# Kernel optimization log

Hardware: AMD Instinct MI355X
Metric: run time of the kernel (lower is better)

## Reference

```python
import jax, jax.numpy as jnp
import numpy as np

EPS = 1e-5

def _bn(x, g, b, m, v):
    # inference-mode batchnorm with moving statistics
    return (x - m) * jax.lax.rsqrt(v + EPS) * g + b

def setup_inputs() -> dict:
    key = jax.random.key(0)
    ks = jax.random.split(key, 12)
    t, b, s, hu = 512, 64, 1024, 1024
    d_in = s + hu
    si = jax.random.normal(ks[0], (b, s), dtype=jnp.float32)
    h = jax.random.normal(ks[1], (t, b, hu), dtype=jnp.float32)
    W0 = jax.random.normal(ks[2], (d_in, 10), dtype=jnp.float32) * 0.02
    b0 = jnp.zeros((10,), jnp.float32)
    g0 = jnp.ones((10,), jnp.float32)
    be0 = jnp.zeros((10,), jnp.float32)
    m0 = jax.random.normal(ks[3], (10,), dtype=jnp.float32) * 0.1
    v0 = jax.random.uniform(ks[4], (10,), dtype=jnp.float32) + 0.5
    W1 = jax.random.normal(ks[5], (10, 5), dtype=jnp.float32) * 0.3
    b1 = jnp.zeros((5,), jnp.float32)
    g1 = jnp.ones((5,), jnp.float32)
    be1 = jnp.zeros((5,), jnp.float32)
    m1 = jax.random.normal(ks[6], (5,), dtype=jnp.float32) * 0.1
    v1 = jax.random.uniform(ks[7], (5,), dtype=jnp.float32) + 0.5
    W2 = jax.random.normal(ks[8], (5, 1), dtype=jnp.float32) * 0.4
    b2 = jnp.zeros((1,), jnp.float32)
    return {"si": si, "h": h, "W0": W0, "b0": b0, "g0": g0, "be0": be0,
            "m0": m0, "v0": v0, "W1": W1, "b1": b1, "g1": g1, "be1": be1,
            "m1": m1, "v1": v1, "W2": W2, "b2": b2}

def reference(si, h, W0, b0, g0, be0, m0, v0, W1, b1, g1, be1, m1, v1, W2, b2):
    t, b, hu = h.shape
    # concat decoder state with every encoder hidden state: [t, b, s+hu]
    x = jnp.concatenate([jnp.broadcast_to(si[None], (t,) + si.shape), h], axis=-1)
    x = jax.nn.relu(_bn(x @ W0 + b0, g0, be0, m0, v0))
    x = jax.nn.relu(_bn(x @ W1 + b1, g1, be1, m1, v1))
    scores = x @ W2 + b2                       # [t, b, 1]
    # original: tf.concat over axis 0 -> [t*b, 1], softmax over axis 0 (ALL t*b entries)
    a = jax.nn.softmax(scores.reshape(t * b))  # [t*b]
    # original uses only the first t rows of the flattened softmax as scalar weights
    ci = jnp.einsum('t,tbh->bh', a[:t], h)     # [b, hu]
    return ci
```

## Files before the change

kernel.cpp:

```cpp
#include <hip/hip_runtime.h>

#define EPS 1e-5f

constexpr int T  = 512;
constexpr int B  = 64;
constexpr int HU = 1024;
constexpr int S  = 1024;
constexpr int P  = T * B;
constexpr int C  = B * HU;
constexpr int TSPLIT = 16;

constexpr size_t OFF_SIW0   = 0;
constexpr size_t OFF_SCORES = 1024;
constexpr size_t OFF_A      = 34816;
constexpr size_t OFF_PART   = 35840;

__global__ __launch_bounds__(256) void k_siw0(const float* __restrict__ si,
                                              const float* __restrict__ W0,
                                              float* __restrict__ out) {
    const int b   = blockIdx.x;
    const int tid = threadIdx.x;
    const float4 sv = ((const float4*)(si + (size_t)b * S))[tid];
    const float* wp = W0 + (size_t)(4 * tid) * 10;

    float acc[10];
#pragma unroll
    for (int j = 0; j < 10; ++j) acc[j] = 0.f;
#pragma unroll
    for (int d = 0; d < 4; ++d) {
        const float hx = (&sv.x)[d];
#pragma unroll
        for (int j = 0; j < 10; ++j) acc[j] = fmaf(hx, wp[d * 10 + j], acc[j]);
    }
#pragma unroll
    for (int j = 0; j < 10; ++j) {
#pragma unroll
        for (int off = 32; off > 0; off >>= 1)
            acc[j] += __shfl_down(acc[j], off, 64);
    }
    __shared__ float red[4][10];
    const int wv = tid >> 6, ln = tid & 63;
    if (ln == 0) {
#pragma unroll
        for (int j = 0; j < 10; ++j) red[wv][j] = acc[j];
    }
    __syncthreads();
    if (tid < 10)
        out[(size_t)b * 10 + tid] =
            red[0][tid] + red[1][tid] + red[2][tid] + red[3][tid];
}

__global__ __launch_bounds__(256) void k_scores(
    const float* __restrict__ h,  const float* __restrict__ W0,
    const float* __restrict__ siW0,
    const float* __restrict__ b0, const float* __restrict__ g0,
    const float* __restrict__ be0,const float* __restrict__ m0,
    const float* __restrict__ v0,
    const float* __restrict__ W1, const float* __restrict__ b1,
    const float* __restrict__ g1, const float* __restrict__ be1,
    const float* __restrict__ m1, const float* __restrict__ v1,
    const float* __restrict__ W2, const float* __restrict__ b2,
    float* __restrict__ scores) {
    const int t   = blockIdx.x;
    const int tid = threadIdx.x;
    const int wv  = tid >> 6;
    const int ln  = tid & 63;
    const int p   = t * 64 + ln;
    const float* hrow = h + (size_t)p * HU;
    const int k0 = __builtin_amdgcn_readfirstlane(wv * 256);

    float acc[10];
#pragma unroll
    for (int j = 0; j < 10; ++j) acc[j] = 0.f;

#pragma unroll 2
    for (int w8 = 0; w8 < 8; ++w8) {
        const int kb = k0 + 32 * w8;
        float4 hv[8];
#pragma unroll
        for (int q = 0; q < 8; ++q)
            hv[q] = *(const float4*)(hrow + kb + 4 * q);
        const float* wp = W0 + (size_t)(1024 + kb) * 10;
#pragma unroll
        for (int q = 0; q < 8; ++q) {
#pragma unroll
            for (int d = 0; d < 4; ++d) {
                const float hx = (&hv[q].x)[d];
#pragma unroll
                for (int j = 0; j < 10; ++j)
                    acc[j] = fmaf(hx, wp[(q * 4 + d) * 10 + j], acc[j]);
            }
        }
    }

    __shared__ float part[4][64][10];
#pragma unroll
    for (int j = 0; j < 10; ++j) part[wv][ln][j] = acc[j];
    __syncthreads();

    if (wv == 0) {
        float y[10];
#pragma unroll
        for (int j = 0; j < 10; ++j) {
            float u = part[0][ln][j] + part[1][ln][j] + part[2][ln][j] +
                      part[3][ln][j] + siW0[(size_t)ln * 10 + j] + b0[j];
            u = (u - m0[j]) * (1.0f / sqrtf(v0[j] + EPS)) * g0[j] + be0[j];
            y[j] = fmaxf(u, 0.f);
        }
        float z[5];
#pragma unroll
        for (int i = 0; i < 5; ++i) {
            float u = b1[i];
#pragma unroll
            for (int j = 0; j < 10; ++j) u = fmaf(y[j], W1[j * 5 + i], u);
            u = (u - m1[i]) * (1.0f / sqrtf(v1[i] + EPS)) * g1[i] + be1[i];
            z[i] = fmaxf(u, 0.f);
        }
        float sc = b2[0];
#pragma unroll
        for (int i = 0; i < 5; ++i) sc = fmaf(z[i], W2[i], sc);
        scores[p] = sc;
    }
}

__global__ __launch_bounds__(1024) void k_softmax(const float* __restrict__ scores,
                                                  float* __restrict__ a) {
    const int tid = threadIdx.x;
    __shared__ float red[16];
    __shared__ float s_m, s_z;

    float v[32];
#pragma unroll
    for (int i = 0; i < 32; ++i) v[i] = scores[tid + i * 1024];

    float mx = v[0];
#pragma unroll
    for (int i = 1; i < 32; ++i) mx = fmaxf(mx, v[i]);
#pragma unroll
    for (int off = 32; off > 0; off >>= 1)
        mx = fmaxf(mx, __shfl_down(mx, off, 64));
    if ((tid & 63) == 0) red[tid >> 6] = mx;
    __syncthreads();
    if (tid == 0) {
        float m = red[0];
        for (int i = 1; i < 16; ++i) m = fmaxf(m, red[i]);
        s_m = m;
    }
    __syncthreads();
    const float m = s_m;

    float sum = 0.f;
#pragma unroll
    for (int i = 0; i < 32; ++i) sum += __expf(v[i] - m);
#pragma unroll
    for (int off = 32; off > 0; off >>= 1)
        sum += __shfl_down(sum, off, 64);
    if ((tid & 63) == 0) red[tid >> 6] = sum;
    __syncthreads();
    if (tid == 0) {
        float z = 0.f;
        for (int i = 0; i < 16; ++i) z += red[i];
        s_z = z;
    }
    __syncthreads();

    if (tid < T) a[tid] = expf(scores[tid] - m) / s_z;
}

__global__ __launch_bounds__(256) void k_wsum(const float* __restrict__ h,
                                              const float* __restrict__ a,
                                              float* __restrict__ part) {
    const int cb = blockIdx.x & 63;
    const int ts = blockIdx.x >> 6;
    const int c  = cb * 1024 + threadIdx.x * 4;
    const float* hp = h + (size_t)ts * 32 * C + c;
    const float* ap = a + ts * 32;

    float4 acc = {0.f, 0.f, 0.f, 0.f};
#pragma unroll 4
    for (int i = 0; i < 32; ++i) {
        const float av = ap[i];
        const float4 hv = *(const float4*)(hp + (size_t)i * C);
        acc.x = fmaf(av, hv.x, acc.x);
        acc.y = fmaf(av, hv.y, acc.y);
        acc.z = fmaf(av, hv.z, acc.z);
        acc.w = fmaf(av, hv.w, acc.w);
    }
    *(float4*)(part + (size_t)ts * C + c) = acc;
}

__global__ __launch_bounds__(256) void k_reduce(const float* __restrict__ part,
                                                float* __restrict__ out) {
    const int c = blockIdx.x * 1024 + threadIdx.x * 4;
    float4 s = {0.f, 0.f, 0.f, 0.f};
#pragma unroll
    for (int ts = 0; ts < TSPLIT; ++ts) {
        const float4 v = *(const float4*)(part + (size_t)ts * C + c);
        s.x += v.x; s.y += v.y; s.z += v.z; s.w += v.w;
    }
    *(float4*)(out + c) = s;
}

extern "C" void kernel_launch(void* const* d_in, const int* in_sizes, int n_in,
                              void* d_out, int out_size, void* d_ws, size_t ws_size,
                              hipStream_t stream) {
    const float* si  = (const float*)d_in[0];
    const float* h   = (const float*)d_in[1];
    const float* W0  = (const float*)d_in[2];
    const float* b0  = (const float*)d_in[3];
    const float* g0  = (const float*)d_in[4];
    const float* be0 = (const float*)d_in[5];
    const float* m0  = (const float*)d_in[6];
    const float* v0  = (const float*)d_in[7];
    const float* W1  = (const float*)d_in[8];
    const float* b1  = (const float*)d_in[9];
    const float* g1  = (const float*)d_in[10];
    const float* be1 = (const float*)d_in[11];
    const float* m1  = (const float*)d_in[12];
    const float* v1  = (const float*)d_in[13];
    const float* W2  = (const float*)d_in[14];
    const float* b2  = (const float*)d_in[15];

    float* ws     = (float*)d_ws;
    float* siW0   = ws + OFF_SIW0;
    float* scores = ws + OFF_SCORES;
    float* a      = ws + OFF_A;
    float* part   = ws + OFF_PART;
    float* out    = (float*)d_out;

    hipLaunchKernelGGL(k_siw0,    dim3(64),   dim3(256),  0, stream, si, W0, siW0);
    hipLaunchKernelGGL(k_scores,  dim3(512),  dim3(256),  0, stream, h, W0, siW0,
                       b0, g0, be0, m0, v0, W1, b1, g1, be1, m1, v1, W2, b2, scores);
    hipLaunchKernelGGL(k_softmax, dim3(1),    dim3(1024), 0, stream, scores, a);
    hipLaunchKernelGGL(k_wsum,    dim3(1024), dim3(256),  0, stream, h, a, part);
    hipLaunchKernelGGL(k_reduce,  dim3(64),   dim3(256),  0, stream, part, out);
}
```

Baseline: 269.5 us.

## Fuse all stages into one cooperative kernel with grid syncs and atomic reduction

Replaces five separate launches with a single cooperative kernel of 512 blocks that computes partial layer-0 products, the si projection, the MLP scores, a two-level softmax (per-block max and sum, then a global combine) and the weighted sum, separated by grid-wide syncs. The weighted-sum partials are accumulated straight into the zeroed output with atomicAdd instead of a partial buffer plus a reduce kernel. This aims to remove launch gaps, the single-block softmax bottleneck and the partial-buffer round trip. In exchange it adds grid-sync overhead and float atomics, it depends on all 512 blocks being co-resident, and the second pass over h may not hit cache after the first.

```diff
diff --git a/kernel.cpp b/kernel.cpp
--- a/kernel.cpp
+++ b/kernel.cpp
@@ -1,4 +1,7 @@
 #include <hip/hip_runtime.h>
+#include <hip/hip_cooperative_groups.h>
+
+namespace cg = cooperative_groups;
 
 #define EPS 1e-5f
 
@@ -6,232 +9,202 @@
 constexpr int B  = 64;
 constexpr int HU = 1024;
 constexpr int S  = 1024;
-constexpr int P  = T * B;
 constexpr int C  = B * HU;
-constexpr int TSPLIT = 16;
-
-constexpr size_t OFF_SIW0   = 0;
-constexpr size_t OFF_SCORES = 1024;
-constexpr size_t OFF_A      = 34816;
-constexpr size_t OFF_PART   = 35840;
-
-__global__ __launch_bounds__(256) void k_siw0(const float* __restrict__ si,
-                                              const float* __restrict__ W0,
-                                              float* __restrict__ out) {
-    const int b   = blockIdx.x;
-    const int tid = threadIdx.x;
-    const float4 sv = ((const float4*)(si + (size_t)b * S))[tid];
-    const float* wp = W0 + (size_t)(4 * tid) * 10;
-
-    float acc[10];
-#pragma unroll
-    for (int j = 0; j < 10; ++j) acc[j] = 0.f;
-#pragma unroll
-    for (int d = 0; d < 4; ++d) {
-        const float hx = (&sv.x)[d];
-#pragma unroll
-        for (int j = 0; j < 10; ++j) acc[j] = fmaf(hx, wp[d * 10 + j], acc[j]);
-    }
-#pragma unroll
-    for (int j = 0; j < 10; ++j) {
-#pragma unroll
-        for (int off = 32; off > 0; off >>= 1)
-            acc[j] += __shfl_down(acc[j], off, 64);
-    }
-    __shared__ float red[4][10];
-    const int wv = tid >> 6, ln = tid & 63;
-    if (ln == 0) {
-#pragma unroll
-        for (int j = 0; j < 10; ++j) red[wv][j] = acc[j];
-    }
-    __syncthreads();
-    if (tid < 10)
-        out[(size_t)b * 10 + tid] =
-            red[0][tid] + red[1][tid] + red[2][tid] + red[3][tid];
-}
-
-__global__ __launch_bounds__(256) void k_scores(
-    const float* __restrict__ h,  const float* __restrict__ W0,
-    const float* __restrict__ siW0,
-    const float* __restrict__ b0, const float* __restrict__ g0,
-    const float* __restrict__ be0,const float* __restrict__ m0,
-    const float* __restrict__ v0,
-    const float* __restrict__ W1, const float* __restrict__ b1,
-    const float* __restrict__ g1, const float* __restrict__ be1,
-    const float* __restrict__ m1, const float* __restrict__ v1,
-    const float* __restrict__ W2, const float* __restrict__ b2,
-    float* __restrict__ scores) {
-    const int t   = blockIdx.x;
+
+constexpr size_t OFF_SIW0 = 0;
+constexpr size_t OFF_BM   = 640;
+constexpr size_t OFF_PZ   = 1152;
+constexpr size_t OFF_A    = 1664;
+
+struct Params {
+    const float *si, *h, *W0, *b0, *g0, *be0, *m0, *v0;
+    const float *W1, *b1, *g1, *be1, *m1, *v1, *W2, *b2;
+    float *ws;
+    float *out;
+};
+
+__global__ __launch_bounds__(256, 2) void k_fused(Params P) {
+    cg::grid_group grid = cg::this_grid();
+    const int bid = blockIdx.x;
     const int tid = threadIdx.x;
     const int wv  = tid >> 6;
     const int ln  = tid & 63;
-    const int p   = t * 64 + ln;
-    const float* hrow = h + (size_t)p * HU;
-    const int k0 = __builtin_amdgcn_readfirstlane(wv * 256);
-
-    float acc[10];
-#pragma unroll
-    for (int j = 0; j < 10; ++j) acc[j] = 0.f;
-
+
+    float* siW0 = P.ws + OFF_SIW0;
+    float* bmv  = P.ws + OFF_BM;
+    float* pzv  = P.ws + OFF_PZ;
+    float* av   = P.ws + OFF_A;
+
+    __shared__ float s_part[4][64][10];
+    __shared__ float s_red[64];
+
+    {
+        const float* hrow = P.h + (size_t)(bid * 64 + ln) * HU;
+        const int k0 = __builtin_amdgcn_readfirstlane(wv * 256);
+        float acc[10];
+#pragma unroll
+        for (int j = 0; j < 10; ++j) acc[j] = 0.f;
 #pragma unroll 2
-    for (int w8 = 0; w8 < 8; ++w8) {
-        const int kb = k0 + 32 * w8;
-        float4 hv[8];
-#pragma unroll
-        for (int q = 0; q < 8; ++q)
-            hv[q] = *(const float4*)(hrow + kb + 4 * q);
-        const float* wp = W0 + (size_t)(1024 + kb) * 10;
-#pragma unroll
-        for (int q = 0; q < 8; ++q) {
-#pragma unroll
-            for (int d = 0; d < 4; ++d) {
-                const float hx = (&hv[q].x)[d];
-#pragma unroll
-                for (int j = 0; j < 10; ++j)
-                    acc[j] = fmaf(hx, wp[(q * 4 + d) * 10 + j], acc[j]);
+        for (int w8 = 0; w8 < 8; ++w8) {
+            const int kb = k0 + 32 * w8;
+            float4 hv[8];
+#pragma unroll
+            for (int q = 0; q < 8; ++q)
+                hv[q] = *(const float4*)(hrow + kb + 4 * q);
+            const float* wp = P.W0 + (size_t)(1024 + kb) * 10;
+#pragma unroll
+            for (int q = 0; q < 8; ++q) {
+#pragma unroll
+                for (int d = 0; d < 4; ++d) {
+                    const float hx = (&hv[q].x)[d];
+#pragma unroll
+                    for (int j = 0; j < 10; ++j)
+                        acc[j] = fmaf(hx, wp[(q * 4 + d) * 10 + j], acc[j]);
+                }
             }
         }
-    }
-
-    __shared__ float part[4][64][10];
-#pragma unroll
-    for (int j = 0; j < 10; ++j) part[wv][ln][j] = acc[j];
-    __syncthreads();
-
+#pragma unroll
+        for (int j = 0; j < 10; ++j) s_part[wv][ln][j] = acc[j];
+    }
+
+    if (bid < 64) {
+        const float4 sv = ((const float4*)(P.si + (size_t)bid * S))[tid];
+        const float* wp = P.W0 + (size_t)(4 * tid) * 10;
+        float sa[10];
+#pragma unroll
+        for (int j = 0; j < 10; ++j) sa[j] = 0.f;
+#pragma unroll
+        for (int d = 0; d < 4; ++d) {
+            const float hx = (&sv.x)[d];
+#pragma unroll
+            for (int j = 0; j < 10; ++j) sa[j] = fmaf(hx, wp[d * 10 + j], sa[j]);
+        }
+#pragma unroll
+        for (int j = 0; j < 10; ++j) {
+#pragma unroll
+            for (int off = 32; off > 0; off >>= 1)
+                sa[j] += __shfl_down(sa[j], off, 64);
+        }
+        __syncthreads();
+        if (ln == 0) {
+#pragma unroll
+            for (int j = 0; j < 10; ++j) s_red[wv * 16 + j] = sa[j];
+        }
+        __syncthreads();
+        if (tid < 10)
+            siW0[(size_t)bid * 10 + tid] = s_red[0 * 16 + tid] + s_red[1 * 16 + tid] +
+                                           s_red[2 * 16 + tid] + s_red[3 * 16 + tid];
+    } else if (bid < 128) {
+        const float4 z4 = {0.f, 0.f, 0.f, 0.f};
+        *(float4*)(P.out + (size_t)(bid - 64) * 1024 + tid * 4) = z4;
+    }
+
+    grid.sync();
+
+    float sc = 0.f;
     if (wv == 0) {
         float y[10];
 #pragma unroll
         for (int j = 0; j < 10; ++j) {
-            float u = part[0][ln][j] + part[1][ln][j] + part[2][ln][j] +
-                      part[3][ln][j] + siW0[(size_t)ln * 10 + j] + b0[j];
-            u = (u - m0[j]) * (1.0f / sqrtf(v0[j] + EPS)) * g0[j] + be0[j];
+            float u = s_part[0][ln][j] + s_part[1][ln][j] + s_part[2][ln][j] +
+                      s_part[3][ln][j] + siW0[(size_t)ln * 10 + j] + P.b0[j];
+            u = (u - P.m0[j]) * (1.0f / sqrtf(P.v0[j] + EPS)) * P.g0[j] + P.be0[j];
             y[j] = fmaxf(u, 0.f);
         }
         float z[5];
 #pragma unroll
         for (int i = 0; i < 5; ++i) {
-            float u = b1[i];
-#pragma unroll
-            for (int j = 0; j < 10; ++j) u = fmaf(y[j], W1[j * 5 + i], u);
-            u = (u - m1[i]) * (1.0f / sqrtf(v1[i] + EPS)) * g1[i] + be1[i];
+            float u = P.b1[i];
+#pragma unroll
+            for (int j = 0; j < 10; ++j) u = fmaf(y[j], P.W1[j * 5 + i], u);
+            u = (u - P.m1[i]) * (1.0f / sqrtf(P.v1[i] + EPS)) * P.g1[i] + P.be1[i];
             z[i] = fmaxf(u, 0.f);
         }
-        float sc = b2[0];
-#pragma unroll
-        for (int i = 0; i < 5; ++i) sc = fmaf(z[i], W2[i], sc);
-        scores[p] = sc;
-    }
-}
-
-__global__ __launch_bounds__(1024) void k_softmax(const float* __restrict__ scores,
-                                                  float* __restrict__ a) {
-    const int tid = threadIdx.x;
-    __shared__ float red[16];
-    __shared__ float s_m, s_z;
-
-    float v[32];
-#pragma unroll
-    for (int i = 0; i < 32; ++i) v[i] = scores[tid + i * 1024];
-
-    float mx = v[0];
-#pragma unroll
-    for (int i = 1; i < 32; ++i) mx = fmaxf(mx, v[i]);
-#pragma unroll
-    for (int off = 32; off > 0; off >>= 1)
-        mx = fmaxf(mx, __shfl_down(mx, off, 64));
-    if ((tid & 63) == 0) red[tid >> 6] = mx;
-    __syncthreads();
-    if (tid == 0) {
-        float m = red[0];
-        for (int i = 1; i < 16; ++i) m = fmaxf(m, red[i]);
-        s_m = m;
-    }
-    __syncthreads();
-    const float m = s_m;
-
-    float sum = 0.f;
-#pragma unroll
-    for (int i = 0; i < 32; ++i) sum += __expf(v[i] - m);
-#pragma unroll
-    for (int off = 32; off > 0; off >>= 1)
-        sum += __shfl_down(sum, off, 64);
-    if ((tid & 63) == 0) red[tid >> 6] = sum;
-    __syncthreads();
-    if (tid == 0) {
-        float z = 0.f;
-        for (int i = 0; i < 16; ++i) z += red[i];
-        s_z = z;
-    }
-    __syncthreads();
-
-    if (tid < T) a[tid] = expf(scores[tid] - m) / s_z;
-}
-
-__global__ __launch_bounds__(256) void k_wsum(const float* __restrict__ h,
-                                              const float* __restrict__ a,
-                                              float* __restrict__ part) {
-    const int cb = blockIdx.x & 63;
-    const int ts = blockIdx.x >> 6;
-    const int c  = cb * 1024 + threadIdx.x * 4;
-    const float* hp = h + (size_t)ts * 32 * C + c;
-    const float* ap = a + ts * 32;
-
-    float4 acc = {0.f, 0.f, 0.f, 0.f};
+        sc = P.b2[0];
+#pragma unroll
+        for (int i = 0; i < 5; ++i) sc = fmaf(z[i], P.W2[i], sc);
+
+        float bm = sc;
+#pragma unroll
+        for (int off = 32; off > 0; off >>= 1)
+            bm = fmaxf(bm, __shfl_xor(bm, off, 64));
+        float e = __expf(sc - bm);
+#pragma unroll
+        for (int off = 32; off > 0; off >>= 1)
+            e += __shfl_xor(e, off, 64);
+        if (ln == 0) { bmv[bid] = bm; pzv[bid] = e; }
+    }
+
+    grid.sync();
+
+    if (bid < 8) {
+        float lm = fmaxf(bmv[tid], bmv[tid + 256]);
+#pragma unroll
+        for (int off = 32; off > 0; off >>= 1)
+            lm = fmaxf(lm, __shfl_xor(lm, off, 64));
+        if (ln == 0) s_red[wv] = lm;
+        __syncthreads();
+        const float m = fmaxf(fmaxf(s_red[0], s_red[1]), fmaxf(s_red[2], s_red[3]));
+        __syncthreads();
+        float lz = pzv[tid] * __expf(bmv[tid] - m) +
+                   pzv[tid + 256] * __expf(bmv[tid + 256] - m);
+#pragma unroll
+        for (int off = 32; off > 0; off >>= 1)
+            lz += __shfl_xor(lz, off, 64);
+        if (ln == 0) s_red[wv] = lz;
+        __syncthreads();
+        const float Z = s_red[0] + s_red[1] + s_red[2] + s_red[3];
+        if (wv == 0) av[bid * 64 + ln] = __expf(sc - m) / Z;
+    }
+
+    grid.sync();
+
+    {
+        const int ts = bid >> 6;
+        const int cb = bid & 63;
+        const int c  = cb * 1024 + tid * 4;
+        const float* hp = P.h + (size_t)ts * 64 * C + c;
+        const float* ap = av + ts * 64;
+        float4 s4 = {0.f, 0.f, 0.f, 0.f};
 #pragma unroll 4
-    for (int i = 0; i < 32; ++i) {
-        const float av = ap[i];
-        const float4 hv = *(const float4*)(hp + (size_t)i * C);
-        acc.x = fmaf(av, hv.x, acc.x);
-        acc.y = fmaf(av, hv.y, acc.y);
-        acc.z = fmaf(av, hv.z, acc.z);
-        acc.w = fmaf(av, hv.w, acc.w);
-    }
-    *(float4*)(part + (size_t)ts * C + c) = acc;
-}
-
-__global__ __launch_bounds__(256) void k_reduce(const float* __restrict__ part,
-                                                float* __restrict__ out) {
-    const int c = blockIdx.x * 1024 + threadIdx.x * 4;
-    float4 s = {0.f, 0.f, 0.f, 0.f};
-#pragma unroll
-    for (int ts = 0; ts < TSPLIT; ++ts) {
-        const float4 v = *(const float4*)(part + (size_t)ts * C + c);
-        s.x += v.x; s.y += v.y; s.z += v.z; s.w += v.w;
-    }
-    *(float4*)(out + c) = s;
+        for (int i = 0; i < 64; ++i) {
+            const float a1 = ap[i];
+            const float4 hv = *(const float4*)(hp + (size_t)i * C);
+            s4.x = fmaf(a1, hv.x, s4.x);
+            s4.y = fmaf(a1, hv.y, s4.y);
+            s4.z = fmaf(a1, hv.z, s4.z);
+            s4.w = fmaf(a1, hv.w, s4.w);
+        }
+        atomicAdd(P.out + c + 0, s4.x);
+        atomicAdd(P.out + c + 1, s4.y);
+        atomicAdd(P.out + c + 2, s4.z);
+        atomicAdd(P.out + c + 3, s4.w);
+    }
 }
 
 extern "C" void kernel_launch(void* const* d_in, const int* in_sizes, int n_in,
                               void* d_out, int out_size, void* d_ws, size_t ws_size,
                               hipStream_t stream) {
-    const float* si  = (const float*)d_in[0];
-    const float* h   = (const float*)d_in[1];
-    const float* W0  = (const float*)d_in[2];
-    const float* b0  = (const float*)d_in[3];
-    const float* g0  = (const float*)d_in[4];
-    const float* be0 = (const float*)d_in[5];
-    const float* m0  = (const float*)d_in[6];
-    const float* v0  = (const float*)d_in[7];
-    const float* W1  = (const float*)d_in[8];
-    const float* b1  = (const float*)d_in[9];
-    const float* g1  = (const float*)d_in[10];
-    const float* be1 = (const float*)d_in[11];
-    const float* m1  = (const float*)d_in[12];
-    const float* v1  = (const float*)d_in[13];
-    const float* W2  = (const float*)d_in[14];
-    const float* b2  = (const float*)d_in[15];
-
-    float* ws     = (float*)d_ws;
-    float* siW0   = ws + OFF_SIW0;
-    float* scores = ws + OFF_SCORES;
-    float* a      = ws + OFF_A;
-    float* part   = ws + OFF_PART;
-    float* out    = (float*)d_out;
-
-    hipLaunchKernelGGL(k_siw0,    dim3(64),   dim3(256),  0, stream, si, W0, siW0);
-    hipLaunchKernelGGL(k_scores,  dim3(512),  dim3(256),  0, stream, h, W0, siW0,
-                       b0, g0, be0, m0, v0, W1, b1, g1, be1, m1, v1, W2, b2, scores);
-    hipLaunchKernelGGL(k_softmax, dim3(1),    dim3(1024), 0, stream, scores, a);
-    hipLaunchKernelGGL(k_wsum,    dim3(1024), dim3(256),  0, stream, h, a, part);
-    hipLaunchKernelGGL(k_reduce,  dim3(64),   dim3(256),  0, stream, part, out);
+    Params p;
+    p.si  = (const float*)d_in[0];
+    p.h   = (const float*)d_in[1];
+    p.W0  = (const float*)d_in[2];
+    p.b0  = (const float*)d_in[3];
+    p.g0  = (const float*)d_in[4];
+    p.be0 = (const float*)d_in[5];
+    p.m0  = (const float*)d_in[6];
+    p.v0  = (const float*)d_in[7];
+    p.W1  = (const float*)d_in[8];
+    p.b1  = (const float*)d_in[9];
+    p.g1  = (const float*)d_in[10];
+    p.be1 = (const float*)d_in[11];
+    p.m1  = (const float*)d_in[12];
+    p.v1  = (const float*)d_in[13];
+    p.W2  = (const float*)d_in[14];
+    p.b2  = (const float*)d_in[15];
+    p.ws  = (float*)d_ws;
+    p.out = (float*)d_out;
+
+    void* args[] = { (void*)&p };
+    hipLaunchCooperativeKernel((void*)k_fused, dim3(512), dim3(256), args, 0, stream);
 }
```

After: 452.3 us. 67.8% more time.

## Stage h tiles through swizzled LDS for coalesced loads in score kernel

Applied to the files above, without the earlier changes.

The score kernel now loads each 64x256 chunk of h cooperatively with fully coalesced float4 reads into a 64 KB shared-memory tile, using an XOR swizzle to avoid bank conflicts. Each lane then reads its own row back from LDS. Before, every lane read its own strided row of h directly from global memory. The change targets poor coalescing on the dominant h read, at the cost of four extra barriers per block, a large LDS footprint that limits occupancy, and less overlap of loads with compute.

```diff
diff --git a/kernel.cpp b/kernel.cpp
--- a/kernel.cpp
+++ b/kernel.cpp
@@ -65,45 +65,54 @@
     const int tid = threadIdx.x;
     const int wv  = tid >> 6;
     const int ln  = tid & 63;
-    const int p   = t * 64 + ln;
-    const float* hrow = h + (size_t)p * HU;
-    const int k0 = __builtin_amdgcn_readfirstlane(wv * 256);
+    const float* hblk = h + (size_t)t * 64 * HU;
+
+    __shared__ float lds[64 * 256];
+    __shared__ float s_part[4][64][10];
 
     float acc[10];
 #pragma unroll
     for (int j = 0; j < 10; ++j) acc[j] = 0.f;
 
-#pragma unroll 2
-    for (int w8 = 0; w8 < 8; ++w8) {
-        const int kb = k0 + 32 * w8;
-        float4 hv[8];
-#pragma unroll
-        for (int q = 0; q < 8; ++q)
-            hv[q] = *(const float4*)(hrow + kb + 4 * q);
-        const float* wp = W0 + (size_t)(1024 + kb) * 10;
-#pragma unroll
-        for (int q = 0; q < 8; ++q) {
+    for (int cc = 0; cc < 4; ++cc) {
+        if (cc) __syncthreads();
+        const float* hc = hblk + cc * 256;
+#pragma unroll
+        for (int it = 0; it < 16; ++it) {
+            const int f = it * 256 + tid;
+            const int r = f >> 6;
+            const int q = f & 63;
+            const float4 v = *(const float4*)(hc + (size_t)r * HU + q * 4);
+            *(float4*)(&lds[r * 256 + ((q ^ r) << 2)]) = v;
+        }
+        __syncthreads();
+        const int qbase = __builtin_amdgcn_readfirstlane(wv * 16);
+#pragma unroll
+        for (int qi = 0; qi < 16; ++qi) {
+            const int qq = qbase + qi;
+            const float4 hv =
+                *(const float4*)(&lds[ln * 256 + ((qq ^ ln) << 2)]);
+            const float* wp = W0 + (size_t)(1024 + cc * 256 + qq * 4) * 10;
 #pragma unroll
             for (int d = 0; d < 4; ++d) {
-                const float hx = (&hv[q].x)[d];
+                const float hx = (&hv.x)[d];
 #pragma unroll
                 for (int j = 0; j < 10; ++j)
-                    acc[j] = fmaf(hx, wp[(q * 4 + d) * 10 + j], acc[j]);
+                    acc[j] = fmaf(hx, wp[d * 10 + j], acc[j]);
             }
         }
     }
 
-    __shared__ float part[4][64][10];
-#pragma unroll
-    for (int j = 0; j < 10; ++j) part[wv][ln][j] = acc[j];
+#pragma unroll
+    for (int j = 0; j < 10; ++j) s_part[wv][ln][j] = acc[j];
     __syncthreads();
 
     if (wv == 0) {
         float y[10];
 #pragma unroll
         for (int j = 0; j < 10; ++j) {
-            float u = part[0][ln][j] + part[1][ln][j] + part[2][ln][j] +
-                      part[3][ln][j] + siW0[(size_t)ln * 10 + j] + b0[j];
+            float u = s_part[0][ln][j] + s_part[1][ln][j] + s_part[2][ln][j] +
+                      s_part[3][ln][j] + siW0[(size_t)ln * 10 + j] + b0[j];
             u = (u - m0[j]) * (1.0f / sqrtf(v0[j] + EPS)) * g0[j] + be0[j];
             y[j] = fmaxf(u, 0.f);
         }
@@ -119,7 +128,7 @@
         float sc = b2[0];
 #pragma unroll
         for (int i = 0; i < 5; ++i) sc = fmaf(z[i], W2[i], sc);
-        scores[p] = sc;
+        scores[t * 64 + ln] = sc;
     }
 }
 
```

Measured after the change: 274.9 us. 2.0% more time.
